# Optimization experiments

Hardware: AMD Instinct MI355X
Metric: run time of the kernel (lower is better)

## Reference

```python
import jax, jax.numpy as jnp
import numpy as np

INPUT_DIM = 256
N_NODES = 100000
N_EDGES = 500000


def setup_inputs() -> dict:
    key = jax.random.key(0)
    ks = jax.random.split(key, 10)
    d = INPUT_DIM

    def linear(kw, kb, fan_in, fan_out):
        # torch nn.Linear default init: U(-1/sqrt(fan_in), 1/sqrt(fan_in))
        bound = 1.0 / np.sqrt(fan_in)
        W = jax.random.uniform(kw, (fan_out, fan_in), jnp.float32, -bound, bound)
        b = jax.random.uniform(kb, (fan_out,), jnp.float32, -bound, bound)
        return W, b

    W1, b1 = linear(ks[0], ks[1], 2 * d, 2 * d)
    W2, b2 = linear(ks[2], ks[3], 2 * d, d)
    W3, b3 = linear(ks[4], ks[5], d, d)
    W4, b4 = linear(ks[6], ks[7], d, 1)

    z = jax.random.normal(ks[8], (N_NODES, d), jnp.float32)
    edge_index = jax.random.randint(ks[9], (2, N_EDGES), 0, N_NODES, jnp.int64)
    return {
        "z": z, "edge_index": edge_index,
        "W1": W1, "b1": b1, "W2": W2, "b2": b2,
        "W3": W3, "b3": b3, "W4": W4, "b4": b4,
    }


def reference(z, edge_index, W1, b1, W2, b2, W3, b3, W4, b4):
    row, col = edge_index[0], edge_index[1]
    # gather endpoint embeddings and concat: [E, 2d]
    z_concat = jnp.concatenate([z[row], z[col]], axis=1)
    # dropout is identity in eval mode (reference runs deterministic)
    x = jax.nn.relu(z_concat @ W1.T + b1)
    x = jax.nn.relu(x @ W2.T + b2)
    x = jax.nn.relu(x @ W3.T + b3)
    return jax.nn.sigmoid(x @ W4.T + b4)  # [E, 1]
```

## Files before the change

kernel.cpp:

```cpp
#include <hip/hip_runtime.h>
#include <math.h>


typedef _Float16 f16x8 __attribute__((ext_vector_type(8)));
typedef _Float16 f16x4 __attribute__((ext_vector_type(4)));
typedef float    f32x4 __attribute__((ext_vector_type(4)));

#define W1E (512*512)
#define W2E (256*512)
#define W3E (256*256)
#define WTOT (W1E+W2E+W3E)
#define H_OFF 1048576

__global__ void repack_w(const float* __restrict__ W1, const float* __restrict__ W2,
                         const float* __restrict__ W3, _Float16* __restrict__ wout) {
  int t = blockIdx.x * 256 + threadIdx.x;
  if (t >= WTOT) return;
  const float* src; _Float16* dst; int K, idx;
  if (t < W1E)            { src = W1; K = 512; idx = t;             dst = wout; }
  else if (t < W1E + W2E) { src = W2; K = 512; idx = t - W1E;       dst = wout + W1E; }
  else                    { src = W3; K = 256; idx = t - (W1E+W2E); dst = wout + W1E + W2E; }
  int j    = idx & 7;
  int lane = (idx >> 3) & 63;
  int rest = idx >> 9;
  int ktiles = K >> 5;
  int kt = rest % ktiles;
  int nt = rest / ktiles;
  int n = nt * 16 + (lane & 15);
  int k = kt * 32 + (lane >> 4) * 8 + j;
  dst[idx] = (_Float16)src[n * K + k];
}

__global__ __launch_bounds__(512, 2)
void precompute_h2(const float* __restrict__ z, int N, const float* __restrict__ b1,
                   const _Float16* __restrict__ w1, _Float16* __restrict__ H) {
  __shared__ char smem[65536];
  const int tid  = threadIdx.x;
  const int wid  = tid >> 6;
  const int lane = tid & 63;
  const int l15  = lane & 15;
  const int lhi  = lane >> 4;
  const int nbase = blockIdx.x * 64;
  const int half = wid >> 2;
  const int wloc = wid & 3;
  char* stg = smem + 32768 + wid * 4096;

  for (int r = wid; r < 64; r += 8) {
    int n = nbase + r; if (n >= N) n = N - 1;
    float4 v = *(const float4*)(z + (size_t)n * 256 + lane * 4);
    f16x4 h;
    h[0] = (_Float16)v.x; h[1] = (_Float16)v.y; h[2] = (_Float16)v.z; h[3] = (_Float16)v.w;
    *(f16x4*)(smem + r * 512 + ((lane * 8) ^ ((r & 7) << 4))) = h;
  }
  __syncthreads();

  for (int p = 0; p < 2; ++p) {
    f32x4 acc[4][4];
    #pragma unroll
    for (int nt = 0; nt < 4; ++nt) {
      f32x4 bv = (f32x4){0.f, 0.f, 0.f, 0.f};
      if (half == 0) bv = *(const f32x4*)(b1 + wloc*128 + p*64 + nt*16 + lhi*4);
      #pragma unroll
      for (int et = 0; et < 4; ++et) acc[nt][et] = bv;
    }

    for (int kt = 0; kt < 8; ++kt) {
      int ktg = kt + half * 8;
      f16x8 wf[4], xf[4];
      #pragma unroll
      for (int nt = 0; nt < 4; ++nt) {
        int ntg = wloc*8 + p*4 + nt;
        wf[nt] = *(const f16x8*)(w1 + (((ntg*16 + ktg)*64 + lane)) * 8);
      }
      #pragma unroll
      for (int et = 0; et < 4; ++et) {
        int r = et*16 + l15;
        xf[et] = *(const f16x8*)(smem + r * 512 + ((kt*64 + lhi*16) ^ ((r & 7) << 4)));
      }
      #pragma unroll
      for (int nt = 0; nt < 4; ++nt)
        #pragma unroll
        for (int et = 0; et < 4; ++et)
          acc[nt][et] = __builtin_amdgcn_mfma_f32_16x16x32_f16(wf[nt], xf[et], acc[nt][et], 0, 0, 0);
    }

    #pragma unroll
    for (int ntp = 0; ntp < 2; ++ntp) {
      #pragma unroll
      for (int nt2 = 0; nt2 < 2; ++nt2) {
        int nt = ntp*2 + nt2;
        #pragma unroll
        for (int et = 0; et < 4; ++et) {
          int node = et*16 + l15;
          f16x4 h;
          #pragma unroll
          for (int r = 0; r < 4; ++r) h[r] = (_Float16)acc[nt][et][r];
          int off = nt2*32 + lhi*8;
          *(f16x4*)(stg + node*64 + (off ^ ((node & 3) << 4))) = h;
        }
      }
      #pragma unroll
      for (int i = 0; i < 4; ++i) {
        int node = i*16 + (lane >> 2);
        int off  = (lane & 3) * 16;
        f16x8 v = *(const f16x8*)(stg + node*64 + (off ^ ((node & 3) << 4)));
        int gn = nbase + node;
        if (gn < N)
          *(f16x8*)(H + (size_t)gn*1024 + half*512 + wloc*128 + p*64 + ntp*32 + (lane & 3)*8) = v;
      }
    }
  }
}

#define SCR_OFF  24576
#define LDS2_BYTES 49152

__global__ __launch_bounds__(512, 6)
void fused_edges48(const int* __restrict__ ei, int E, const _Float16* __restrict__ H,
                   const float* __restrict__ b2, const float* __restrict__ b3,
                   const float* __restrict__ W4, const float* __restrict__ b4,
                   const _Float16* __restrict__ w2, const _Float16* __restrict__ w3,
                   float* __restrict__ out) {
  extern __shared__ char smem[];
  float* scr = (float*)(smem + SCR_OFF);

  const int tid  = threadIdx.x;
  const int wid  = tid >> 6;
  const int lane = tid & 63;
  const int l15  = lane & 15;
  const int lhi  = lane >> 4;
  const int base = blockIdx.x * 48;

  #pragma unroll 3
  for (int e = wid; e < 48; e += 8) {
    int ge = base + e; if (ge >= E) ge = E - 1;
    int nr = ei[ge];
    int nc = ei[E + ge];
    f16x8 ha = *(const f16x8*)(H + (size_t)nr * 1024 + lane * 8);
    f16x8 hb = *(const f16x8*)(H + (size_t)nc * 1024 + 512 + lane * 8);
    f16x8 s = ha + hb;
    #pragma unroll
    for (int j = 0; j < 8; ++j) s[j] = (s[j] > (_Float16)0) ? s[j] : (_Float16)0;
    *(f16x8*)(smem + e * 1024 + ((lane * 16) ^ ((e & 7) << 4))) = s;
  }
  __syncthreads();

  f32x4 acc2[2][3];
  #pragma unroll
  for (int nt = 0; nt < 2; ++nt) {
    f32x4 bv = *(const f32x4*)(b2 + wid*32 + nt*16 + lhi*4);
    #pragma unroll
    for (int et = 0; et < 3; ++et) acc2[nt][et] = bv;
  }
  #pragma unroll 2
  for (int kt = 0; kt < 16; ++kt) {
    f16x8 wf[2], xf[3];
    #pragma unroll
    for (int nt = 0; nt < 2; ++nt)
      wf[nt] = *(const f16x8*)(w2 + (((wid*2 + nt)*16 + kt)*64 + lane) * 8);
    #pragma unroll
    for (int et = 0; et < 3; ++et) {
      int e = et*16 + l15;
      xf[et] = *(const f16x8*)(smem + e * 1024 + ((kt*64 + lhi*16) ^ ((e & 7) << 4)));
    }
    #pragma unroll
    for (int nt = 0; nt < 2; ++nt)
      #pragma unroll
      for (int et = 0; et < 3; ++et)
        acc2[nt][et] = __builtin_amdgcn_mfma_f32_16x16x32_f16(wf[nt], xf[et], acc2[nt][et], 0, 0, 0);
  }
  __syncthreads();
  #pragma unroll
  for (int nt = 0; nt < 2; ++nt)
    #pragma unroll
    for (int et = 0; et < 3; ++et) {
      int e = et*16 + l15;
      int ncb = (wid*32 + nt*16 + lhi*4) * 2;
      f16x4 h;
      #pragma unroll
      for (int r = 0; r < 4; ++r) h[r] = (_Float16)fmaxf(acc2[nt][et][r], 0.f);
      *(f16x4*)(smem + e * 512 + (ncb ^ ((e & 7) << 4))) = h;
    }
  __syncthreads();

  f32x4 acc3[2][3];
  #pragma unroll
  for (int nt = 0; nt < 2; ++nt) {
    f32x4 bv = *(const f32x4*)(b3 + wid*32 + nt*16 + lhi*4);
    #pragma unroll
    for (int et = 0; et < 3; ++et) acc3[nt][et] = bv;
  }
  #pragma unroll 2
  for (int kt = 0; kt < 8; ++kt) {
    f16x8 wf[2], xf[3];
    #pragma unroll
    for (int nt = 0; nt < 2; ++nt)
      wf[nt] = *(const f16x8*)(w3 + (((wid*2 + nt)*8 + kt)*64 + lane) * 8);
    #pragma unroll
    for (int et = 0; et < 3; ++et) {
      int e = et*16 + l15;
      xf[et] = *(const f16x8*)(smem + e * 512 + ((kt*64 + lhi*16) ^ ((e & 7) << 4)));
    }
    #pragma unroll
    for (int nt = 0; nt < 2; ++nt)
      #pragma unroll
      for (int et = 0; et < 3; ++et)
        acc3[nt][et] = __builtin_amdgcn_mfma_f32_16x16x32_f16(wf[nt], xf[et], acc3[nt][et], 0, 0, 0);
  }

  f32x4 w4v[2];
  #pragma unroll
  for (int nt = 0; nt < 2; ++nt)
    w4v[nt] = *(const f32x4*)(W4 + wid*32 + nt*16 + lhi*4);

  #pragma unroll
  for (int et = 0; et < 3; ++et) {
    float p = 0.f;
    #pragma unroll
    for (int nt = 0; nt < 2; ++nt)
      #pragma unroll
      for (int r = 0; r < 4; ++r)
        p += fmaxf(acc3[nt][et][r], 0.f) * w4v[nt][r];
    p += __shfl_xor(p, 16);
    p += __shfl_xor(p, 32);
    if (lane < 16) scr[(et*16 + l15) * 8 + wid] = p;
  }
  __syncthreads();

  if (tid < 48) {
    int ge = base + tid;
    if (ge < E) {
      float s = b4[0];
      #pragma unroll
      for (int w = 0; w < 8; ++w) s += scr[tid*8 + w];
      out[ge] = 1.f / (1.f + expf(-s));
    }
  }
}

#define FSCR_OFF  65536
#define FBIAS_OFF 67584
#define FLDS_BYTES 72832

__global__ __launch_bounds__(512, 2)
void fused_fallback(const float* __restrict__ z, const int* __restrict__ ei, int E,
                    const float* __restrict__ b1, const float* __restrict__ b2,
                    const float* __restrict__ b3, const float* __restrict__ W4,
                    const float* __restrict__ b4,
                    const _Float16* __restrict__ wbuf, float* __restrict__ out) {
  extern __shared__ char smem[];
  float* scr = (float*)(smem + FSCR_OFF);
  float* bls = (float*)(smem + FBIAS_OFF);

  const int tid  = threadIdx.x;
  const int wid  = tid >> 6;
  const int lane = tid & 63;
  const int l15  = lane & 15;
  const int lhi  = lane >> 4;
  const int base = blockIdx.x * 64;

  for (int i = tid; i < 1281; i += 512) {
    float v;
    if (i < 512)       v = b1[i];
    else if (i < 768)  v = b2[i - 512];
    else if (i < 1024) v = b3[i - 768];
    else if (i < 1280) v = W4[i - 1024];
    else               v = b4[0];
    bls[i] = v;
  }

  for (int it = wid; it < 128; it += 8) {
    int e = it >> 1, hf = it & 1;
    int ge = base + e; if (ge >= E) ge = E - 1;
    int src = ei[hf ? (E + ge) : ge];
    float4 v = *(const float4*)(z + (size_t)src * 256 + lane * 4);
    f16x4 h;
    h[0] = (_Float16)v.x; h[1] = (_Float16)v.y; h[2] = (_Float16)v.z; h[3] = (_Float16)v.w;
    *(f16x4*)(smem + e * 1024 + ((hf * 512 + lane * 8) ^ ((e & 7) << 4))) = h;
  }
  __syncthreads();

  const _Float16* w1 = wbuf;
  const _Float16* w2 = wbuf + W1E;
  const _Float16* w3 = wbuf + W1E + W2E;

  f32x4 acc1[4][4];
  #pragma unroll
  for (int nt = 0; nt < 4; ++nt) {
    f32x4 bv = *(const f32x4*)(bls + wid*64 + nt*16 + lhi*4);
    #pragma unroll
    for (int et = 0; et < 4; ++et) acc1[nt][et] = bv;
  }
  for (int kt = 0; kt < 16; ++kt) {
    f16x8 wf[4], xf[4];
    #pragma unroll
    for (int nt = 0; nt < 4; ++nt)
      wf[nt] = *(const f16x8*)(w1 + (((wid*4 + nt)*16 + kt)*64 + lane) * 8);
    #pragma unroll
    for (int et = 0; et < 4; ++et) {
      int e = et*16 + l15;
      xf[et] = *(const f16x8*)(smem + e * 1024 + ((kt*64 + lhi*16) ^ ((e & 7) << 4)));
    }
    #pragma unroll
    for (int nt = 0; nt < 4; ++nt)
      #pragma unroll
      for (int et = 0; et < 4; ++et)
        acc1[nt][et] = __builtin_amdgcn_mfma_f32_16x16x32_f16(wf[nt], xf[et], acc1[nt][et], 0, 0, 0);
  }
  __syncthreads();
  #pragma unroll
  for (int nt = 0; nt < 4; ++nt)
    #pragma unroll
    for (int et = 0; et < 4; ++et) {
      int e = et*16 + l15;
      int ncb = (wid*64 + nt*16 + lhi*4) * 2;
      f16x4 h;
      #pragma unroll
      for (int r = 0; r < 4; ++r) h[r] = (_Float16)fmaxf(acc1[nt][et][r], 0.f);
      *(f16x4*)(smem + e * 1024 + (ncb ^ ((e & 7) << 4))) = h;
    }
  __syncthreads();

  f32x4 acc2[2][4];
  #pragma unroll
  for (int nt = 0; nt < 2; ++nt) {
    f32x4 bv = *(const f32x4*)(bls + 512 + wid*32 + nt*16 + lhi*4);
    #pragma unroll
    for (int et = 0; et < 4; ++et) acc2[nt][et] = bv;
  }
  for (int kt = 0; kt < 16; ++kt) {
    f16x8 wf[2], xf[4];
    #pragma unroll
    for (int nt = 0; nt < 2; ++nt)
      wf[nt] = *(const f16x8*)(w2 + (((wid*2 + nt)*16 + kt)*64 + lane) * 8);
    #pragma unroll
    for (int et = 0; et < 4; ++et) {
      int e = et*16 + l15;
      xf[et] = *(const f16x8*)(smem + e * 1024 + ((kt*64 + lhi*16) ^ ((e & 7) << 4)));
    }
    #pragma unroll
    for (int nt = 0; nt < 2; ++nt)
      #pragma unroll
      for (int et = 0; et < 4; ++et)
        acc2[nt][et] = __builtin_amdgcn_mfma_f32_16x16x32_f16(wf[nt], xf[et], acc2[nt][et], 0, 0, 0);
  }
  __syncthreads();
  #pragma unroll
  for (int nt = 0; nt < 2; ++nt)
    #pragma unroll
    for (int et = 0; et < 4; ++et) {
      int e = et*16 + l15;
      int ncb = (wid*32 + nt*16 + lhi*4) * 2;
      f16x4 h;
      #pragma unroll
      for (int r = 0; r < 4; ++r) h[r] = (_Float16)fmaxf(acc2[nt][et][r], 0.f);
      *(f16x4*)(smem + e * 512 + (ncb ^ ((e & 7) << 4))) = h;
    }
  __syncthreads();

  f32x4 acc3[2][4];
  #pragma unroll
  for (int nt = 0; nt < 2; ++nt) {
    f32x4 bv = *(const f32x4*)(bls + 768 + wid*32 + nt*16 + lhi*4);
    #pragma unroll
    for (int et = 0; et < 4; ++et) acc3[nt][et] = bv;
  }
  for (int kt = 0; kt < 8; ++kt) {
    f16x8 wf[2], xf[4];
    #pragma unroll
    for (int nt = 0; nt < 2; ++nt)
      wf[nt] = *(const f16x8*)(w3 + (((wid*2 + nt)*8 + kt)*64 + lane) * 8);
    #pragma unroll
    for (int et = 0; et < 4; ++et) {
      int e = et*16 + l15;
      xf[et] = *(const f16x8*)(smem + e * 512 + ((kt*64 + lhi*16) ^ ((e & 7) << 4)));
    }
    #pragma unroll
    for (int nt = 0; nt < 2; ++nt)
      #pragma unroll
      for (int et = 0; et < 4; ++et)
        acc3[nt][et] = __builtin_amdgcn_mfma_f32_16x16x32_f16(wf[nt], xf[et], acc3[nt][et], 0, 0, 0);
  }

  f32x4 w4v[2];
  #pragma unroll
  for (int nt = 0; nt < 2; ++nt)
    w4v[nt] = *(const f32x4*)(bls + 1024 + wid*32 + nt*16 + lhi*4);
  float bias4 = bls[1280];

  #pragma unroll
  for (int et = 0; et < 4; ++et) {
    float p = 0.f;
    #pragma unroll
    for (int nt = 0; nt < 2; ++nt)
      #pragma unroll
      for (int r = 0; r < 4; ++r)
        p += fmaxf(acc3[nt][et][r], 0.f) * w4v[nt][r];
    p += __shfl_xor(p, 16);
    p += __shfl_xor(p, 32);
    if (lane < 16) scr[(et*16 + l15) * 8 + wid] = p;
  }
  __syncthreads();

  if (tid < 64) {
    int ge = base + tid;
    if (ge < E) {
      float s = bias4;
      #pragma unroll
      for (int w = 0; w < 8; ++w) s += scr[tid*8 + w];
      out[ge] = 1.f / (1.f + expf(-s));
    }
  }
}

extern "C" void kernel_launch(void* const* d_in, const int* in_sizes, int n_in,
                              void* d_out, int out_size, void* d_ws, size_t ws_size,
                              hipStream_t stream) {
  const float* z  = (const float*)d_in[0];
  const int*   ei = (const int*)d_in[1];
  const float* W1 = (const float*)d_in[2];
  const float* b1 = (const float*)d_in[3];
  const float* W2 = (const float*)d_in[4];
  const float* b2 = (const float*)d_in[5];
  const float* W3 = (const float*)d_in[6];
  const float* b3 = (const float*)d_in[7];
  const float* W4 = (const float*)d_in[8];
  const float* b4 = (const float*)d_in[9];
  float* out = (float*)d_out;
  const int E = in_sizes[1] / 2;
  const int N = in_sizes[0] / 256;

  _Float16* wbuf = (_Float16*)d_ws;
  _Float16* H    = (_Float16*)((char*)d_ws + H_OFF);

  repack_w<<<(WTOT + 255) / 256, 256, 0, stream>>>(W1, W2, W3, wbuf);

  size_t need = (size_t)H_OFF + (size_t)N * 1024 * 2;
  if (ws_size >= need) {
    precompute_h2<<<(N + 63) / 64, 512, 0, stream>>>(z, N, b1, wbuf, H);
    int nblk = (E + 47) / 48;
    fused_edges48<<<nblk, 512, LDS2_BYTES, stream>>>(ei, E, H, b2, b3, W4, b4,
                                                     wbuf + W1E, wbuf + W1E + W2E, out);
  } else {
    int nblk = (E + 63) / 64;
    fused_fallback<<<nblk, 512, FLDS_BYTES, stream>>>(z, ei, E, b1, b2, b3, W4, b4, wbuf, out);
  }
}
```

Before: 409.2 us.

## Make edge MLP kernel persistent with software-pipelined gather of next tile

Turns the per-tile edge kernel into a persistent kernel over a fixed grid of 512 blocks. Each block loops over tiles and issues the edge-index loads and H-row gathers for the next tile while the current tile's layer-2/3 MFMAs run. The layer-2 output gets its own LDS region so the gathered inputs are not overwritten. This is meant to hide gather latency behind compute, at the cost of more LDS, lower occupancy (4 blocks/CU hint) and extra registers for the prefetched rows.

```diff
diff --git a/kernel.cpp b/kernel.cpp
--- a/kernel.cpp
+++ b/kernel.cpp
@@ -112,11 +112,13 @@
   }
 }
 
-#define SCR_OFF  24576
-#define LDS2_BYTES 49152
-
-__global__ __launch_bounds__(512, 6)
-void fused_edges48(const int* __restrict__ ei, int E, const _Float16* __restrict__ H,
+#define X2_OFF  49152
+#define SCR_OFF 73728
+#define LDSP_BYTES 75264
+
+__global__ __launch_bounds__(512, 4)
+void fused_edges_p(const int* __restrict__ ei, int E, int ntiles,
+                   const _Float16* __restrict__ H,
                    const float* __restrict__ b2, const float* __restrict__ b3,
                    const float* __restrict__ W4, const float* __restrict__ b4,
                    const _Float16* __restrict__ w2, const _Float16* __restrict__ w3,
@@ -129,112 +131,151 @@
   const int lane = tid & 63;
   const int l15  = lane & 15;
   const int lhi  = lane >> 4;
-  const int base = blockIdx.x * 48;
-
-  #pragma unroll 3
-  for (int e = wid; e < 48; e += 8) {
-    int ge = base + e; if (ge >= E) ge = E - 1;
-    int nr = ei[ge];
-    int nc = ei[E + ge];
-    f16x8 ha = *(const f16x8*)(H + (size_t)nr * 1024 + lane * 8);
-    f16x8 hb = *(const f16x8*)(H + (size_t)nc * 1024 + 512 + lane * 8);
-    f16x8 s = ha + hb;
+
+  int tile = blockIdx.x;
+
+  f16x8 ha_s[6], hb_s[6];
+  #pragma unroll
+  for (int i = 0; i < 6; ++i) {
+    int ge = tile*48 + i*8 + wid; if (ge >= E) ge = E - 1;
+    int nr = ei[ge], nc = ei[E + ge];
+    ha_s[i] = *(const f16x8*)(H + (size_t)nr*1024 + lane*8);
+    hb_s[i] = *(const f16x8*)(H + (size_t)nc*1024 + 512 + lane*8);
+  }
+  #pragma unroll
+  for (int i = 0; i < 6; ++i) {
+    int e = i*8 + wid;
+    f16x8 s = ha_s[i] + hb_s[i];
     #pragma unroll
     for (int j = 0; j < 8; ++j) s[j] = (s[j] > (_Float16)0) ? s[j] : (_Float16)0;
-    *(f16x8*)(smem + e * 1024 + ((lane * 16) ^ ((e & 7) << 4))) = s;
-  }
-  __syncthreads();
-
-  f32x4 acc2[2][3];
-  #pragma unroll
-  for (int nt = 0; nt < 2; ++nt) {
-    f32x4 bv = *(const f32x4*)(b2 + wid*32 + nt*16 + lhi*4);
-    #pragma unroll
-    for (int et = 0; et < 3; ++et) acc2[nt][et] = bv;
-  }
-  #pragma unroll 2
-  for (int kt = 0; kt < 16; ++kt) {
-    f16x8 wf[2], xf[3];
-    #pragma unroll
-    for (int nt = 0; nt < 2; ++nt)
-      wf[nt] = *(const f16x8*)(w2 + (((wid*2 + nt)*16 + kt)*64 + lane) * 8);
+    *(f16x8*)(smem + e*1024 + ((lane*16) ^ ((e & 7) << 4))) = s;
+  }
+  __syncthreads();
+
+  for (;;) {
+    const int next = tile + gridDim.x;
+    const bool has_next = (next < ntiles);
+
+    int eir[6], eic[6];
+    if (has_next) {
+      #pragma unroll
+      for (int i = 0; i < 6; ++i) {
+        int ge = next*48 + i*8 + wid; if (ge >= E) ge = E - 1;
+        eir[i] = ei[ge]; eic[i] = ei[E + ge];
+      }
+    }
+
+    f32x4 acc2[2][3];
+    #pragma unroll
+    for (int nt = 0; nt < 2; ++nt) {
+      f32x4 bv = *(const f32x4*)(b2 + wid*32 + nt*16 + lhi*4);
+      #pragma unroll
+      for (int et = 0; et < 3; ++et) acc2[nt][et] = bv;
+    }
+    for (int kt = 0; kt < 16; ++kt) {
+      f16x8 wf[2], xf[3];
+      #pragma unroll
+      for (int nt = 0; nt < 2; ++nt)
+        wf[nt] = *(const f16x8*)(w2 + (((wid*2 + nt)*16 + kt)*64 + lane) * 8);
+      #pragma unroll
+      for (int et = 0; et < 3; ++et) {
+        int e = et*16 + l15;
+        xf[et] = *(const f16x8*)(smem + e*1024 + ((kt*64 + lhi*16) ^ ((e & 7) << 4)));
+      }
+      #pragma unroll
+      for (int nt = 0; nt < 2; ++nt)
+        #pragma unroll
+        for (int et = 0; et < 3; ++et)
+          acc2[nt][et] = __builtin_amdgcn_mfma_f32_16x16x32_f16(wf[nt], xf[et], acc2[nt][et], 0, 0, 0);
+    }
+    #pragma unroll
+    for (int nt = 0; nt < 2; ++nt)
+      #pragma unroll
+      for (int et = 0; et < 3; ++et) {
+        int e = et*16 + l15;
+        int ncb = (wid*32 + nt*16 + lhi*4) * 2;
+        f16x4 h;
+        #pragma unroll
+        for (int r = 0; r < 4; ++r) h[r] = (_Float16)fmaxf(acc2[nt][et][r], 0.f);
+        *(f16x4*)(smem + X2_OFF + e*512 + (ncb ^ ((e & 7) << 4))) = h;
+      }
+    __syncthreads();
+
+    f32x4 acc3[2][3];
+    #pragma unroll
+    for (int nt = 0; nt < 2; ++nt) {
+      f32x4 bv = *(const f32x4*)(b3 + wid*32 + nt*16 + lhi*4);
+      #pragma unroll
+      for (int et = 0; et < 3; ++et) acc3[nt][et] = bv;
+    }
+    for (int kt = 0; kt < 8; ++kt) {
+      f16x8 wf[2], xf[3];
+      #pragma unroll
+      for (int nt = 0; nt < 2; ++nt)
+        wf[nt] = *(const f16x8*)(w3 + (((wid*2 + nt)*8 + kt)*64 + lane) * 8);
+      #pragma unroll
+      for (int et = 0; et < 3; ++et) {
+        int e = et*16 + l15;
+        xf[et] = *(const f16x8*)(smem + X2_OFF + e*512 + ((kt*64 + lhi*16) ^ ((e & 7) << 4)));
+      }
+      #pragma unroll
+      for (int nt = 0; nt < 2; ++nt)
+        #pragma unroll
+        for (int et = 0; et < 3; ++et)
+          acc3[nt][et] = __builtin_amdgcn_mfma_f32_16x16x32_f16(wf[nt], xf[et], acc3[nt][et], 0, 0, 0);
+    }
+
+    __builtin_amdgcn_sched_barrier(0);
+    if (has_next) {
+      #pragma unroll
+      for (int i = 0; i < 6; ++i) {
+        ha_s[i] = *(const f16x8*)(H + (size_t)eir[i]*1024 + lane*8);
+        hb_s[i] = *(const f16x8*)(H + (size_t)eic[i]*1024 + 512 + lane*8);
+      }
+    }
+    __builtin_amdgcn_sched_barrier(0);
+
+    f32x4 w4v[2];
+    #pragma unroll
+    for (int nt = 0; nt < 2; ++nt)
+      w4v[nt] = *(const f32x4*)(W4 + wid*32 + nt*16 + lhi*4);
+
     #pragma unroll
     for (int et = 0; et < 3; ++et) {
-      int e = et*16 + l15;
-      xf[et] = *(const f16x8*)(smem + e * 1024 + ((kt*64 + lhi*16) ^ ((e & 7) << 4)));
-    }
-    #pragma unroll
-    for (int nt = 0; nt < 2; ++nt)
-      #pragma unroll
-      for (int et = 0; et < 3; ++et)
-        acc2[nt][et] = __builtin_amdgcn_mfma_f32_16x16x32_f16(wf[nt], xf[et], acc2[nt][et], 0, 0, 0);
-  }
-  __syncthreads();
-  #pragma unroll
-  for (int nt = 0; nt < 2; ++nt)
-    #pragma unroll
-    for (int et = 0; et < 3; ++et) {
-      int e = et*16 + l15;
-      int ncb = (wid*32 + nt*16 + lhi*4) * 2;
-      f16x4 h;
-      #pragma unroll
-      for (int r = 0; r < 4; ++r) h[r] = (_Float16)fmaxf(acc2[nt][et][r], 0.f);
-      *(f16x4*)(smem + e * 512 + (ncb ^ ((e & 7) << 4))) = h;
-    }
-  __syncthreads();
-
-  f32x4 acc3[2][3];
-  #pragma unroll
-  for (int nt = 0; nt < 2; ++nt) {
-    f32x4 bv = *(const f32x4*)(b3 + wid*32 + nt*16 + lhi*4);
-    #pragma unroll
-    for (int et = 0; et < 3; ++et) acc3[nt][et] = bv;
-  }
-  #pragma unroll 2
-  for (int kt = 0; kt < 8; ++kt) {
-    f16x8 wf[2], xf[3];
-    #pragma unroll
-    for (int nt = 0; nt < 2; ++nt)
-      wf[nt] = *(const f16x8*)(w3 + (((wid*2 + nt)*8 + kt)*64 + lane) * 8);
-    #pragma unroll
-    for (int et = 0; et < 3; ++et) {
-      int e = et*16 + l15;
-      xf[et] = *(const f16x8*)(smem + e * 512 + ((kt*64 + lhi*16) ^ ((e & 7) << 4)));
-    }
-    #pragma unroll
-    for (int nt = 0; nt < 2; ++nt)
-      #pragma unroll
-      for (int et = 0; et < 3; ++et)
-        acc3[nt][et] = __builtin_amdgcn_mfma_f32_16x16x32_f16(wf[nt], xf[et], acc3[nt][et], 0, 0, 0);
-  }
-
-  f32x4 w4v[2];
-  #pragma unroll
-  for (int nt = 0; nt < 2; ++nt)
-    w4v[nt] = *(const f32x4*)(W4 + wid*32 + nt*16 + lhi*4);
-
-  #pragma unroll
-  for (int et = 0; et < 3; ++et) {
-    float p = 0.f;
-    #pragma unroll
-    for (int nt = 0; nt < 2; ++nt)
-      #pragma unroll
-      for (int r = 0; r < 4; ++r)
-        p += fmaxf(acc3[nt][et][r], 0.f) * w4v[nt][r];
-    p += __shfl_xor(p, 16);
-    p += __shfl_xor(p, 32);
-    if (lane < 16) scr[(et*16 + l15) * 8 + wid] = p;
-  }
-  __syncthreads();
-
-  if (tid < 48) {
-    int ge = base + tid;
-    if (ge < E) {
-      float s = b4[0];
-      #pragma unroll
-      for (int w = 0; w < 8; ++w) s += scr[tid*8 + w];
-      out[ge] = 1.f / (1.f + expf(-s));
-    }
+      float p = 0.f;
+      #pragma unroll
+      for (int nt = 0; nt < 2; ++nt)
+        #pragma unroll
+        for (int r = 0; r < 4; ++r)
+          p += fmaxf(acc3[nt][et][r], 0.f) * w4v[nt][r];
+      p += __shfl_xor(p, 16);
+      p += __shfl_xor(p, 32);
+      if (lane < 16) scr[(et*16 + l15) * 8 + wid] = p;
+    }
+    __syncthreads();
+
+    if (tid < 48) {
+      int ge = tile*48 + tid;
+      if (ge < E) {
+        float s = b4[0];
+        #pragma unroll
+        for (int w = 0; w < 8; ++w) s += scr[tid*8 + w];
+        out[ge] = 1.f / (1.f + expf(-s));
+      }
+    }
+
+    if (!has_next) return;
+
+    #pragma unroll
+    for (int i = 0; i < 6; ++i) {
+      int e = i*8 + wid;
+      f16x8 s = ha_s[i] + hb_s[i];
+      #pragma unroll
+      for (int j = 0; j < 8; ++j) s[j] = (s[j] > (_Float16)0) ? s[j] : (_Float16)0;
+      *(f16x8*)(smem + e*1024 + ((lane*16) ^ ((e & 7) << 4))) = s;
+    }
+    __syncthreads();
+    tile = next;
   }
 }
 
@@ -438,8 +479,9 @@
   size_t need = (size_t)H_OFF + (size_t)N * 1024 * 2;
   if (ws_size >= need) {
     precompute_h2<<<(N + 63) / 64, 512, 0, stream>>>(z, N, b1, wbuf, H);
-    int nblk = (E + 47) / 48;
-    fused_edges48<<<nblk, 512, LDS2_BYTES, stream>>>(ei, E, H, b2, b3, W4, b4,
+    int ntiles = (E + 47) / 48;
+    int nblk = ntiles < 512 ? ntiles : 512;
+    fused_edges_p<<<nblk, 512, LDSP_BYTES, stream>>>(ei, E, ntiles, H, b2, b3, W4, b4,
                                                      wbuf + W1E, wbuf + W1E + W2E, out);
   } else {
     int nblk = (E + 63) / 64;
```

Result: slower. 1.612 ms (+293.9%).
